# Kernel tuning notes

Hardware: AMD Instinct MI355X
Metric: run time of the kernel (lower is better)

## Reference

```python
import jax, jax.numpy as jnp
import numpy as np

B, M, D = 4096, 200, 100          # batch, max_neighbor, embed_dim
NSYM, NENT = 100001, 5000         # num_symbols+1, num_entities


def setup_inputs() -> dict:
    key = jax.random.key(0)
    ks = jax.random.split(key, 12)
    s = 0.05  # weight init scale to keep activations sane
    return {
        "connections": jax.random.randint(ks[0], (B, M, 3), 0, NENT),
        "target": jax.random.randint(ks[1], (B, 1, 2), 0, NENT),
        "symbol_emb": jax.random.normal(ks[2], (NSYM, D), jnp.float32),
        "co_entities": jax.random.uniform(ks[3], (NENT, NENT), dtype=jnp.float32),
        "gcn_w_weight": jax.random.normal(ks[4], (D, 2 * D), jnp.float32) * s,
        "gcn_w_bias": jax.random.normal(ks[5], (D,), jnp.float32) * s,
        "gcn_b": jnp.zeros((D,), jnp.float32),
        "attn_w_weight": jax.random.normal(ks[6], (1, D), jnp.float32) * s,
        "attn_w_bias": jnp.zeros((1,), jnp.float32),
        "gate_w_weight": jax.random.normal(ks[7], (1, D), jnp.float32) * s,
        "gate_w_bias": jnp.zeros((1,), jnp.float32),
        "gate_b": jnp.zeros((1,), jnp.float32),
    }


def reference(connections, target, symbol_emb, co_entities,
              gcn_w_weight, gcn_w_bias, gcn_b,
              attn_w_weight, attn_w_bias,
              gate_w_weight, gate_w_bias, gate_b):
    # --- neighbor gather ---
    relations = connections[:, :, 1]            # [B, M]
    entities = connections[:, :, 2]             # [B, M]
    entself = connections[:, 0, 0]              # [B]
    rel_embeds = symbol_emb[relations]          # [B, M, D]
    ent_embeds = symbol_emb[entities]           # [B, M, D]
    entself_embeds = symbol_emb[entself]        # [B, D]

    # co-occurrence weights: co[b, m] = co_entities[entities[b,m], target_ent[b]]
    target_ent = target[:, 0, 0]                # [B]
    co_weight = co_entities[entities, target_ent[:, None]]  # [B, M]

    # --- linear + leaky_relu (gcn) ---
    concat = jnp.concatenate([rel_embeds, ent_embeds], axis=-1)   # [B, M, 2D]
    out = jnp.einsum('bmk,dk->bmd', concat, gcn_w_weight) + gcn_w_bias + gcn_b
    out = jax.nn.leaky_relu(out, negative_slope=0.01)             # [B, M, D]

    # --- attention over neighbors ---
    attn_out = jnp.einsum('bmd,od->bmo', out, attn_w_weight) + attn_w_bias  # [B, M, 1]
    attn_weight = jax.nn.softmax(attn_out, axis=1)
    out_attn = jnp.einsum('bmd,bmo->bd', out, attn_weight)        # [B, D]

    # --- sigmoid gate ---
    gate = jax.nn.sigmoid(out_attn @ gate_w_weight.T + gate_w_bias + gate_b)  # [B, 1]
    out_neigh = out_attn * gate

    # --- co-weighted neighbor aggregation ---
    neighbor_emb = jnp.einsum('bm,bmd->bd', co_weight, ent_embeds)  # [B, D]

    return out_neigh + entself_embeds * (1.0 - gate) + neighbor_emb
```

## Files before the change

### kernel.cpp

```cpp
#include <hip/hip_runtime.h>

#define BB   4096
#define MM   200
#define DD   100
#define NENT 5000
#define LPW  30
#define PTW  101

typedef _Float16 f16x2 __attribute__((ext_vector_type(2)));
typedef unsigned uint2v __attribute__((ext_vector_type(2)));

#if defined(__has_builtin)
#if __has_builtin(__builtin_amdgcn_fdot2)
#define HAS_FDOT2 1
#endif
#endif

__device__ __forceinline__ f16x2 uh(unsigned u) { return __builtin_bit_cast(f16x2, u); }
__device__ __forceinline__ float2 h2f(f16x2 h) { return make_float2((float)h.x, (float)h.y); }


__global__ __launch_bounds__(256) void precompute_kernel(
    const float* __restrict__ sym, const float* __restrict__ W,
    const float* __restrict__ wb, const float* __restrict__ gb,
    _Float16* __restrict__ Pr, _Float16* __restrict__ PES)
{
    __shared__ _Float16 Wt[200 * 102];
    const int tid = threadIdx.x;
    for (int j = tid; j < 20000; j += 256) {
        int d = j / 200, k = j % 200;
        Wt[k * 102 + d] = (_Float16)W[j];
    }
    __syncthreads();

    const int i = blockIdx.x * 256 + tid;
    if (i >= NENT * 50) return;
    const int e = i / 50, dp = i % 50;
    const float* se = sym + e * DD;

    float pr0 = 0.f, pr1 = 0.f, pe0 = 0.f, pe1 = 0.f;
    for (int k = 0; k < 100; k++) {
        float a = se[k];
        f16x2 w01 = *(const f16x2*)&Wt[k * 102 + 2 * dp];
        f16x2 w23 = *(const f16x2*)&Wt[(k + 100) * 102 + 2 * dp];
        pr0 = fmaf(a, (float)w01.x, pr0);
        pr1 = fmaf(a, (float)w01.y, pr1);
        pe0 = fmaf(a, (float)w23.x, pe0);
        pe1 = fmaf(a, (float)w23.y, pe1);
    }
    const int d0 = 2 * dp;
    pr0 += wb[d0]     + gb[d0];
    pr1 += wb[d0 + 1] + gb[d0 + 1];

    *(f16x2*)&Pr[e * DD + d0]           = f16x2{(_Float16)pr0, (_Float16)pr1};
    *(f16x2*)&PES[e * 2 * DD + d0]      = f16x2{(_Float16)pe0, (_Float16)pe1};
    *(f16x2*)&PES[e * 2 * DD + DD + d0] = f16x2{(_Float16)se[d0], (_Float16)se[d0 + 1]};
}

__global__ __launch_bounds__(256, 4) void main_kernel(
    const int*  __restrict__ conn, const int* __restrict__ target,
    const float* __restrict__ sym, const float* __restrict__ co,
    const _Float16* __restrict__ Pr, const _Float16* __restrict__ PES,
    const float* __restrict__ attn_w,
    const float* __restrict__ gate_w, const float* __restrict__ gate_wb,
    const float* __restrict__ gate_b,
    float* __restrict__ outp)
{
    __shared__ __align__(16) unsigned char scratch_raw[MM * LPW * 2];
    __shared__ unsigned idx_s[MM];
    __shared__ float    co_s[MM];
    __shared__ float    ev_s[MM];
    __shared__ float    red[8];
    _Float16* lp_s = (_Float16*)scratch_raw;
    float*    part = (float*)scratch_raw;

    const int t = threadIdx.x;
    const int b = blockIdx.x;
    const int* cb = conn + b * (MM * 3);
    const int lane = t & 63, wid = t >> 6;

    float co_reg = 0.f;
    if (t < MM) {
        int r = cb[t * 3 + 1];
        int e = cb[t * 3 + 2];
        idx_s[t] = (unsigned)r | ((unsigned)e << 16);
        int tgt = target[b * 2];
        co_reg = co[(long)e * NENT + tgt];
    }
    __syncthreads();

    const int g = t / 25, dq = t % 25;
    const bool act = (t < 250);

    float4 awf = *(const float4*)&attn_w[4 * dq];
#ifdef HAS_FDOT2
    f16x2 aw01 = f16x2{(_Float16)awf.x, (_Float16)awf.y};
    f16x2 aw23 = f16x2{(_Float16)awf.z, (_Float16)awf.w};
#endif
    const _Float16 slope = (_Float16)0.01f;

    uint2v xs[20];

    if (act) {
        #pragma unroll
        for (int it = 0; it < 20; ++it) {
            int m = g + 10 * it;
            unsigned ir = idx_s[m];
            int r = ir & 0xffff, e = ir >> 16;
            uint2v pru = *(const uint2v*)(Pr + r * DD + 4 * dq);
            uint2v peu = *(const uint2v*)(PES + e * 2 * DD + 4 * dq);
            f16x2 x01 = uh(pru.x) + uh(peu.x);
            f16x2 x23 = uh(pru.y) + uh(peu.y);
            x01 = __builtin_elementwise_max(x01, x01 * slope);
            x23 = __builtin_elementwise_max(x23, x23 * slope);
            xs[it].x = __builtin_bit_cast(unsigned, x01);
            xs[it].y = __builtin_bit_cast(unsigned, x23);
            float lp;
#ifdef HAS_FDOT2
            lp = __builtin_amdgcn_fdot2(x01, aw01, 0.0f, false);
            lp = __builtin_amdgcn_fdot2(x23, aw23, lp, false);
#else
            float2 f01 = h2f(x01), f23 = h2f(x23);
            lp = f01.x * awf.x + f01.y * awf.y + f23.x * awf.z + f23.y * awf.w;
#endif
            lp_s[m * LPW + dq] = (_Float16)lp;
        }
    }
    __syncthreads();

    float logit = 0.f;
    if (t < MM) {
        const _Float16* row = lp_s + t * LPW;
        const unsigned* rw = (const unsigned*)row;
        float acc0 = 0.f, acc1 = 0.f, acc2 = 0.f, acc3 = 0.f;
        #pragma unroll
        for (int i = 0; i < 12; i += 4) {
            float2 a = h2f(uh(rw[i]));
            float2 b2 = h2f(uh(rw[i + 1]));
            float2 c = h2f(uh(rw[i + 2]));
            float2 d = h2f(uh(rw[i + 3]));
            acc0 += a.x + a.y;
            acc1 += b2.x + b2.y;
            acc2 += c.x + c.y;
            acc3 += d.x + d.y;
        }
        logit = (acc0 + acc1) + (acc2 + acc3) + (float)row[24];
    }

    float ev = (t < MM) ? __expf(logit) : 0.f;
    if (t < MM) {
        ev_s[t] = ev;
        co_s[t] = co_reg;
    }
    float s = ev;
    for (int off = 32; off >= 1; off >>= 1) s += __shfl_xor(s, off);
    if (lane == 0) red[4 + wid] = s;
    __syncthreads();
    float gsum = (red[4] + red[5]) + (red[6] + red[7]);

    float oa0 = 0.f, oa1 = 0.f, oa2 = 0.f, oa3 = 0.f;
    f16x2 nb01 = f16x2{(_Float16)0.f, (_Float16)0.f};
    f16x2 nb23 = nb01;
    if (act) {
        #pragma unroll
        for (int it = 0; it < 20; ++it) {
            int m = g + 10 * it;
            float w = ev_s[m];
            float2 f01 = h2f(uh(xs[it].x));
            float2 f23 = h2f(uh(xs[it].y));
            oa0 = fmaf(w, f01.x, oa0);
            oa1 = fmaf(w, f01.y, oa1);
            oa2 = fmaf(w, f23.x, oa2);
            oa3 = fmaf(w, f23.y, oa3);
            int e = idx_s[m] >> 16;
            uint2v syu = *(const uint2v*)(PES + e * 2 * DD + DD + 4 * dq);
            _Float16 coh = (_Float16)co_s[m];
            f16x2 co2 = f16x2{coh, coh};
            nb01 = co2 * uh(syu.x) + nb01;
            nb23 = co2 * uh(syu.y) + nb23;
        }
    }
    float inv = 1.f / gsum;
    oa0 *= inv; oa1 *= inv; oa2 *= inv; oa3 *= inv;

    if (act) {
        float* po = &part[g * PTW + 4 * dq];
        po[0] = oa0; po[1] = oa1; po[2] = oa2; po[3] = oa3;
        float2 n01 = h2f(nb01), n23 = h2f(nb23);
        float* pn = &part[(10 + g) * PTW + 4 * dq];
        pn[0] = n01.x; pn[1] = n01.y; pn[2] = n23.x; pn[3] = n23.y;
    }
    __syncthreads();

    float oaf = 0.f, nbf = 0.f;
    if (t < DD) {
        #pragma unroll
        for (int g2 = 0; g2 < 10; ++g2) {
            oaf += part[g2 * PTW + t];
            nbf += part[(10 + g2) * PTW + t];
        }
    }

    float p = (t < DD) ? oaf * gate_w[t] : 0.f;
    for (int off = 32; off >= 1; off >>= 1) p += __shfl_xor(p, off);
    if (lane == 0) red[wid] = p;
    __syncthreads();
    float dot = (red[0] + red[1]) + (red[2] + red[3]);
    float gt = 1.f / (1.f + __expf(-(dot + gate_wb[0] + gate_b[0])));

    if (t < DD) {
        float self_v = sym[cb[0] * DD + t];
        outp[b * DD + t] = oaf * gt + self_v * (1.f - gt) + nbf;
    }
}

extern "C" void kernel_launch(void* const* d_in, const int* in_sizes, int n_in,
                              void* d_out, int out_size, void* d_ws, size_t ws_size,
                              hipStream_t stream) {
    const int*   conn    = (const int*)  d_in[0];
    const int*   target  = (const int*)  d_in[1];
    const float* sym     = (const float*)d_in[2];
    const float* co      = (const float*)d_in[3];
    const float* W       = (const float*)d_in[4];
    const float* wb      = (const float*)d_in[5];
    const float* gb      = (const float*)d_in[6];
    const float* attn_w  = (const float*)d_in[7];
    const float* gate_w  = (const float*)d_in[9];
    const float* gate_wb = (const float*)d_in[10];
    const float* gate_b  = (const float*)d_in[11];

    _Float16* Pr  = (_Float16*)d_ws;
    _Float16* PES = (_Float16*)((char*)d_ws + 1000000);

    precompute_kernel<<<(NENT * 50 + 255) / 256, 256, 0, stream>>>(
        sym, W, wb, gb, Pr, PES);

    main_kernel<<<BB, 256, 0, stream>>>(
        conn, target, sym, co, Pr, PES,
        attn_w, gate_w, gate_wb, gate_b, (float*)d_out);
}
```

Baseline: 67.17 us.

## Process neighbors in two chunks to cut registers and LDS, raise occupancy

The 200-neighbor loop is split into two chunks of 100. Each chunk runs its own gather, logit reduction, softmax partial sum and weighted accumulation, so the per-thread register buffer shrinks from 20 to 10 entries and the shared logit scratch halves. Launch bounds now ask for 6 blocks per CU instead of 4, giving more waves to hide gather latency. The cost is an extra pair of barriers and reductions per block, and less memory-level parallelism within each wave.

```diff
diff --git a/kernel.cpp b/kernel.cpp
--- a/kernel.cpp
+++ b/kernel.cpp
@@ -4,6 +4,7 @@
 #define MM   200
 #define DD   100
 #define NENT 5000
+#define CH   100
 #define LPW  30
 #define PTW  101
 
@@ -57,7 +58,7 @@
     *(f16x2*)&PES[e * 2 * DD + DD + d0] = f16x2{(_Float16)se[d0], (_Float16)se[d0 + 1]};
 }
 
-__global__ __launch_bounds__(256, 4) void main_kernel(
+__global__ __launch_bounds__(256, 6) void main_kernel(
     const int*  __restrict__ conn, const int* __restrict__ target,
     const float* __restrict__ sym, const float* __restrict__ co,
     const _Float16* __restrict__ Pr, const _Float16* __restrict__ PES,
@@ -66,7 +67,7 @@
     const float* __restrict__ gate_b,
     float* __restrict__ outp)
 {
-    __shared__ __align__(16) unsigned char scratch_raw[MM * LPW * 2];
+    __shared__ __align__(16) unsigned char scratch_raw[2 * 10 * PTW * 4];
     __shared__ unsigned idx_s[MM];
     __shared__ float    co_s[MM];
     __shared__ float    ev_s[MM];
@@ -99,85 +100,88 @@
 #endif
     const _Float16 slope = (_Float16)0.01f;
 
-    uint2v xs[20];
-
-    if (act) {
-        #pragma unroll
-        for (int it = 0; it < 20; ++it) {
-            int m = g + 10 * it;
-            unsigned ir = idx_s[m];
-            int r = ir & 0xffff, e = ir >> 16;
-            uint2v pru = *(const uint2v*)(Pr + r * DD + 4 * dq);
-            uint2v peu = *(const uint2v*)(PES + e * 2 * DD + 4 * dq);
-            f16x2 x01 = uh(pru.x) + uh(peu.x);
-            f16x2 x23 = uh(pru.y) + uh(peu.y);
-            x01 = __builtin_elementwise_max(x01, x01 * slope);
-            x23 = __builtin_elementwise_max(x23, x23 * slope);
-            xs[it].x = __builtin_bit_cast(unsigned, x01);
-            xs[it].y = __builtin_bit_cast(unsigned, x23);
-            float lp;
-#ifdef HAS_FDOT2
-            lp = __builtin_amdgcn_fdot2(x01, aw01, 0.0f, false);
-            lp = __builtin_amdgcn_fdot2(x23, aw23, lp, false);
-#else
-            float2 f01 = h2f(x01), f23 = h2f(x23);
-            lp = f01.x * awf.x + f01.y * awf.y + f23.x * awf.z + f23.y * awf.w;
-#endif
-            lp_s[m * LPW + dq] = (_Float16)lp;
-        }
-    }
-    __syncthreads();
-
-    float logit = 0.f;
-    if (t < MM) {
-        const _Float16* row = lp_s + t * LPW;
-        const unsigned* rw = (const unsigned*)row;
-        float acc0 = 0.f, acc1 = 0.f, acc2 = 0.f, acc3 = 0.f;
-        #pragma unroll
-        for (int i = 0; i < 12; i += 4) {
-            float2 a = h2f(uh(rw[i]));
-            float2 b2 = h2f(uh(rw[i + 1]));
-            float2 c = h2f(uh(rw[i + 2]));
-            float2 d = h2f(uh(rw[i + 3]));
-            acc0 += a.x + a.y;
-            acc1 += b2.x + b2.y;
-            acc2 += c.x + c.y;
-            acc3 += d.x + d.y;
-        }
-        logit = (acc0 + acc1) + (acc2 + acc3) + (float)row[24];
-    }
-
-    float ev = (t < MM) ? __expf(logit) : 0.f;
-    if (t < MM) {
-        ev_s[t] = ev;
-        co_s[t] = co_reg;
-    }
-    float s = ev;
-    for (int off = 32; off >= 1; off >>= 1) s += __shfl_xor(s, off);
-    if (lane == 0) red[4 + wid] = s;
-    __syncthreads();
-    float gsum = (red[4] + red[5]) + (red[6] + red[7]);
-
     float oa0 = 0.f, oa1 = 0.f, oa2 = 0.f, oa3 = 0.f;
     f16x2 nb01 = f16x2{(_Float16)0.f, (_Float16)0.f};
     f16x2 nb23 = nb01;
-    if (act) {
-        #pragma unroll
-        for (int it = 0; it < 20; ++it) {
-            int m = g + 10 * it;
-            float w = ev_s[m];
-            float2 f01 = h2f(uh(xs[it].x));
-            float2 f23 = h2f(uh(xs[it].y));
-            oa0 = fmaf(w, f01.x, oa0);
-            oa1 = fmaf(w, f01.y, oa1);
-            oa2 = fmaf(w, f23.x, oa2);
-            oa3 = fmaf(w, f23.y, oa3);
-            int e = idx_s[m] >> 16;
-            uint2v syu = *(const uint2v*)(PES + e * 2 * DD + DD + 4 * dq);
-            _Float16 coh = (_Float16)co_s[m];
-            f16x2 co2 = f16x2{coh, coh};
-            nb01 = co2 * uh(syu.x) + nb01;
-            nb23 = co2 * uh(syu.y) + nb23;
+    float gsum = 0.f;
+
+    for (int c = 0; c < 2; ++c) {
+        uint2v xs[10];
+
+        if (act) {
+            #pragma unroll
+            for (int it = 0; it < 10; ++it) {
+                int ml = g + 10 * it;
+                int m = c * CH + ml;
+                unsigned ir = idx_s[m];
+                int r = ir & 0xffff, e = ir >> 16;
+                uint2v pru = *(const uint2v*)(Pr + r * DD + 4 * dq);
+                uint2v peu = *(const uint2v*)(PES + e * 2 * DD + 4 * dq);
+                f16x2 x01 = uh(pru.x) + uh(peu.x);
+                f16x2 x23 = uh(pru.y) + uh(peu.y);
+                x01 = __builtin_elementwise_max(x01, x01 * slope);
+                x23 = __builtin_elementwise_max(x23, x23 * slope);
+                xs[it].x = __builtin_bit_cast(unsigned, x01);
+                xs[it].y = __builtin_bit_cast(unsigned, x23);
+                float lp;
+#ifdef HAS_FDOT2
+                lp = __builtin_amdgcn_fdot2(x01, aw01, 0.0f, false);
+                lp = __builtin_amdgcn_fdot2(x23, aw23, lp, false);
+#else
+                float2 f01 = h2f(x01), f23 = h2f(x23);
+                lp = f01.x * awf.x + f01.y * awf.y + f23.x * awf.z + f23.y * awf.w;
+#endif
+                lp_s[ml * LPW + dq] = (_Float16)lp;
+            }
+        }
+        __syncthreads();
+
+        float ev = 0.f;
+        if (t < CH) {
+            const _Float16* row = lp_s + t * LPW;
+            const unsigned* rw = (const unsigned*)row;
+            float acc0 = 0.f, acc1 = 0.f, acc2 = 0.f, acc3 = 0.f;
+            #pragma unroll
+            for (int i = 0; i < 12; i += 4) {
+                float2 a = h2f(uh(rw[i]));
+                float2 b2 = h2f(uh(rw[i + 1]));
+                float2 cc = h2f(uh(rw[i + 2]));
+                float2 d = h2f(uh(rw[i + 3]));
+                acc0 += a.x + a.y;
+                acc1 += b2.x + b2.y;
+                acc2 += cc.x + cc.y;
+                acc3 += d.x + d.y;
+            }
+            float logit = (acc0 + acc1) + (acc2 + acc3) + (float)row[24];
+            ev = __expf(logit);
+            ev_s[c * CH + t] = ev;
+        }
+        if (c == 0 && t < MM) co_s[t] = co_reg;
+        float s = ev;
+        for (int off = 32; off >= 1; off >>= 1) s += __shfl_xor(s, off);
+        if (lane == 0) red[4 + wid] = s;
+        __syncthreads();
+        gsum += (red[4] + red[5]) + (red[6] + red[7]);
+
+        if (act) {
+            #pragma unroll
+            for (int it = 0; it < 10; ++it) {
+                int ml = g + 10 * it;
+                int m = c * CH + ml;
+                float w = ev_s[m];
+                float2 f01 = h2f(uh(xs[it].x));
+                float2 f23 = h2f(uh(xs[it].y));
+                oa0 = fmaf(w, f01.x, oa0);
+                oa1 = fmaf(w, f01.y, oa1);
+                oa2 = fmaf(w, f23.x, oa2);
+                oa3 = fmaf(w, f23.y, oa3);
+                int e = idx_s[m] >> 16;
+                uint2v syu = *(const uint2v*)(PES + e * 2 * DD + DD + 4 * dq);
+                _Float16 coh = (_Float16)co_s[m];
+                f16x2 co2 = f16x2{coh, coh};
+                nb01 = co2 * uh(syu.x) + nb01;
+                nb23 = co2 * uh(syu.y) + nb23;
+            }
         }
     }
     float inv = 1.f / gsum;
```

New measurement: 68.99 us. +2.7%, slower.
